# Kernel optimization log

Hardware: AMD Instinct MI355X
Metric: run time of the kernel (lower is better)

Reference implementation:

```python
import jax, jax.numpy as jnp
import numpy as np

B, S, E, H, U = 2048, 64, 512, 512, 512

def setup_inputs() -> dict:
    key = jax.random.key(0)
    ks = jax.random.split(key, 6)
    s = lambda d: 1.0 / np.sqrt(d)
    return {
        "features": jax.random.normal(ks[0], (B, S, E), jnp.float32),
        "hidden": jax.random.normal(ks[1], (B, H), jnp.float32),
        "W1": jax.random.normal(ks[2], (E, U), jnp.float32) * s(E),
        "b1": jnp.zeros((U,), jnp.float32),
        "W2": jax.random.normal(ks[3], (H, U), jnp.float32) * s(H),
        "b2": jnp.zeros((U,), jnp.float32),
        "Wv": jax.random.normal(ks[4], (U, 1), jnp.float32) * s(U),
        "bv": jnp.zeros((1,), jnp.float32),
    }

def reference(features, hidden, W1, b1, W2, b2, Wv, bv):
    # Bahdanau additive attention (dropout at inference = identity).
    h1 = jnp.einsum('bse,eu->bsu', features, W1) + b1          # [B,S,U]
    h2 = hidden @ W2 + b2                                       # [B,U]
    scores = jnp.tanh(h1 + h2[:, None, :]) @ Wv + bv            # [B,S,1]
    weights = jax.nn.softmax(scores, axis=1)                    # softmax over seq
    context = jnp.sum(weights * features, axis=1)               # [B,E]
    return context
```

## Files before the change

### kernel.cpp

```cpp
#include <hip/hip_runtime.h>

typedef _Float16 f16x8 __attribute__((ext_vector_type(8)));
typedef unsigned short u16x4 __attribute__((ext_vector_type(4)));
typedef float f32x4 __attribute__((ext_vector_type(4)));

#define VMWAIT(N) asm volatile("s_waitcnt vmcnt(" #N ")" ::: "memory")

__global__ void convert_w_kernel(const float* __restrict__ w1,
                                 const float* __restrict__ w2,
                                 unsigned short* __restrict__ w1img,
                                 unsigned short* __restrict__ w2img) {
    int u = blockIdx.x;
    int k = threadIdx.x + blockIdx.y * 256;
    size_t idx = (size_t)(k >> 5) * 16384 + (size_t)u * 32 + (k & 31);
    _Float16 h1 = (_Float16)w1[(size_t)k * 512 + u];
    _Float16 h2 = (_Float16)w2[(size_t)k * 512 + u];
    w1img[idx] = __builtin_bit_cast(unsigned short, h1);
    w2img[idx] = __builtin_bit_cast(unsigned short, h2);
}

__device__ __forceinline__ void stage_a64(const float* __restrict__ src,
                                          char* As, int tid) {
    const int row = tid >> 2, q = tid & 3;
    const float* p = src + (size_t)row * 512 + q * 4;
    const int sw2 = ((row >> 1) & 3) << 4;
    char* wb = As + row * 64;
    float4 va[4], vb[4];
#define AISS(V, G) { _Pragma("unroll") \
    for (int j_ = 0; j_ < 4; ++j_) V[j_] = *(const float4*)(p + ((G) * 4 + j_) * 16); }
#define APRC(V, G) { _Pragma("unroll") \
    for (int j_ = 0; j_ < 4; ++j_) { \
        const int i_ = (G) * 4 + j_; \
        u16x4 h_; \
        h_[0] = __builtin_bit_cast(unsigned short, (_Float16)V[j_].x); \
        h_[1] = __builtin_bit_cast(unsigned short, (_Float16)V[j_].y); \
        h_[2] = __builtin_bit_cast(unsigned short, (_Float16)V[j_].z); \
        h_[3] = __builtin_bit_cast(unsigned short, (_Float16)V[j_].w); \
        *(u16x4*)(wb + (i_ >> 1) * 4096 + ((q * 8 + (i_ & 1) * 32) ^ sw2)) = h_; } }
    AISS(va, 0); AISS(vb, 1);
    VMWAIT(4); APRC(va, 0); AISS(va, 2);
    VMWAIT(4); APRC(vb, 1); AISS(vb, 3);
    VMWAIT(4); APRC(va, 2); AISS(va, 4);
    VMWAIT(4); APRC(vb, 3); AISS(vb, 5);
    VMWAIT(4); APRC(va, 4); AISS(va, 6);
    VMWAIT(4); APRC(vb, 5); AISS(vb, 7);
    VMWAIT(4); APRC(va, 6);
    VMWAIT(0); APRC(vb, 7);
#undef AISS
#undef APRC
}

__device__ __forceinline__ void chunk_gemm(const char* __restrict__ bcol,
                                           const char* As, const int* aoff,
                                           f32x4 acc[4][4]) {
    f16x8 brA[4], brB[4], afA[4], afB[4];
    #pragma unroll
    for (int i = 0; i < 4; ++i)
        #pragma unroll
        for (int j = 0; j < 4; ++j) acc[i][j] = (f32x4){0.f, 0.f, 0.f, 0.f};
    #pragma unroll
    for (int j = 0; j < 4; ++j) brA[j] = *(const f16x8*)(bcol + j * 1024);
    #pragma unroll
    for (int j = 0; j < 4; ++j) brB[j] = *(const f16x8*)(bcol + 32768 + j * 1024);
    #pragma unroll
    for (int i = 0; i < 4; ++i) afA[i] = *(const f16x8*)(As + aoff[i]);

    #pragma unroll
    for (int tt = 0; tt < 8; ++tt) {
        const int t0 = 2 * tt, t1 = t0 + 1;
        if (t0 < 15) {
            #pragma unroll
            for (int i = 0; i < 4; ++i)
                afB[i] = *(const f16x8*)(As + t1 * 4096 + aoff[i]);
        }
        VMWAIT(4);
        #pragma unroll
        for (int i = 0; i < 4; ++i)
            #pragma unroll
            for (int j = 0; j < 4; ++j)
                acc[i][j] = __builtin_amdgcn_mfma_f32_16x16x32_f16(afA[i], brA[j], acc[i][j], 0, 0, 0);
        if (t0 < 14) {
            #pragma unroll
            for (int j = 0; j < 4; ++j)
                brA[j] = *(const f16x8*)(bcol + (t0 + 2) * 32768 + j * 1024);
        }
        if (t1 < 15) {
            #pragma unroll
            for (int i = 0; i < 4; ++i)
                afA[i] = *(const f16x8*)(As + (t1 + 1) * 4096 + aoff[i]);
        }
        if (t1 < 14) { VMWAIT(4); } else { VMWAIT(0); }
        #pragma unroll
        for (int i = 0; i < 4; ++i)
            #pragma unroll
            for (int j = 0; j < 4; ++j)
                acc[i][j] = __builtin_amdgcn_mfma_f32_16x16x32_f16(afB[i], brB[j], acc[i][j], 0, 0, 0);
        if (t1 < 14) {
            #pragma unroll
            for (int j = 0; j < 4; ++j)
                brB[j] = *(const f16x8*)(bcol + (t1 + 2) * 32768 + j * 1024);
        }
    }
}

__global__ __launch_bounds__(256, 2)
void h2_gemm_kernel(const float* __restrict__ hidden,
                    const char* __restrict__ w2img,
                    const float* __restrict__ b2,
                    float* __restrict__ h2o) {
    __shared__ char As[65536];
    const int tid = threadIdx.x, bm = blockIdx.x;
    const int lane = tid & 63, wid = tid >> 6;
    const int lane16 = lane & 15, g = lane >> 4;
    stage_a64(hidden + (size_t)bm * 32768, As, tid);
    __syncthreads();
    const int swA = (lane16 >> 1) & 3;
    int aoff[4];
    #pragma unroll
    for (int i = 0; i < 4; ++i)
        aoff[i] = (i * 16 + lane16) * 64 + ((g ^ swA) << 4);
    #pragma unroll
    for (int c = 0; c < 2; ++c) {
        const char* bcol = w2img + (size_t)(wid * 128 + c * 64 + lane16) * 64 + g * 16;
        f32x4 acc[4][4];
        chunk_gemm(bcol, As, aoff, acc);
        #pragma unroll
        for (int j = 0; j < 4; ++j) {
            int col = wid * 128 + c * 64 + j * 16 + lane16;
            float bb = b2[col];
            #pragma unroll
            for (int i = 0; i < 4; ++i)
                #pragma unroll
                for (int r = 0; r < 4; ++r)
                    h2o[(size_t)(bm * 64 + i * 16 + g * 4 + r) * 512 + col] = acc[i][j][r] + bb;
        }
    }
}

__global__ __launch_bounds__(256, 2)
void fused_all_kernel(const float* __restrict__ feat,
                      const char* __restrict__ w1img,
                      const float* __restrict__ h2,
                      const float* __restrict__ b1,
                      const float* __restrict__ wv,
                      float* __restrict__ out) {
    __shared__ char As[65536];
    __shared__ float spl[256];
    __shared__ float wsm[64];
    const int tid = threadIdx.x, bm = blockIdx.x;
    const int lane = tid & 63, wid = tid >> 6;
    const int lane16 = lane & 15, g = lane >> 4;

    stage_a64(feat + (size_t)bm * 32768, As, tid);
    __syncthreads();

    float hhv[8], wvv[8];
    #pragma unroll
    for (int j = 0; j < 8; ++j) {
        int u = wid * 128 + j * 16 + lane16;
        hhv[j] = b1[u] + h2[(size_t)bm * 512 + u];
        wvv[j] = wv[u];
    }
    VMWAIT(0);

    const int swA = (lane16 >> 1) & 3;
    int aoff[4];
    #pragma unroll
    for (int i = 0; i < 4; ++i)
        aoff[i] = (i * 16 + lane16) * 64 + ((g ^ swA) << 4);

    float sacc[16];
    #pragma unroll
    for (int x = 0; x < 16; ++x) sacc[x] = 0.f;

    #pragma unroll
    for (int c = 0; c < 2; ++c) {
        const char* bcol = w1img + (size_t)(wid * 128 + c * 64 + lane16) * 64 + g * 16;
        f32x4 acc[4][4];
        chunk_gemm(bcol, As, aoff, acc);
        #pragma unroll
        for (int i = 0; i < 4; ++i)
            #pragma unroll
            for (int r = 0; r < 4; ++r) {
                float s = 0.f;
                #pragma unroll
                for (int j = 0; j < 4; ++j) {
                    float h = acc[i][j][r] + hhv[c * 4 + j];
                    float ex = __expf(2.f * h);
                    s += (1.f - 2.f * __builtin_amdgcn_rcpf(ex + 1.f)) * wvv[c * 4 + j];
                }
                sacc[i * 4 + r] += s;
            }
    }

    #pragma unroll
    for (int i = 0; i < 4; ++i)
        #pragma unroll
        for (int r = 0; r < 4; ++r) {
            float s = sacc[i * 4 + r];
            s += __shfl_xor(s, 1); s += __shfl_xor(s, 2);
            s += __shfl_xor(s, 4); s += __shfl_xor(s, 8);
            if (lane16 == 0) spl[(i * 16 + g * 4 + r) * 4 + wid] = s;
        }
    __syncthreads();

    if (tid < 64) {
        float s = (spl[tid * 4 + 0] + spl[tid * 4 + 1]) +
                  (spl[tid * 4 + 2] + spl[tid * 4 + 3]);
        float m = s;
        #pragma unroll
        for (int off = 32; off; off >>= 1) m = fmaxf(m, __shfl_xor(m, off));
        float e = __expf(s - m);
        float sum = e;
        #pragma unroll
        for (int off = 32; off; off >>= 1) sum += __shfl_xor(sum, off);
        wsm[tid] = e / sum;
    }
    __syncthreads();

    {
        const int cseg = (tid >> 4) * 4096;
        const int cin = (tid & 15) * 4;
        float ax = 0.f, ay = 0.f;
        #pragma unroll 8
        for (int s = 0; s < 64; ++s) {
            unsigned v = *(const unsigned*)(As + cseg + s * 64 +
                                            (cin ^ (((s >> 1) & 3) << 4)));
            float w = wsm[s];
            ax += w * (float)__builtin_bit_cast(_Float16, (unsigned short)(v & 0xffffu));
            ay += w * (float)__builtin_bit_cast(_Float16, (unsigned short)(v >> 16));
        }
        ((float2*)out)[(size_t)bm * 256 + tid] = make_float2(ax, ay);
    }
}

extern "C" void kernel_launch(void* const* d_in, const int* in_sizes, int n_in,
                              void* d_out, int out_size, void* d_ws, size_t ws_size,
                              hipStream_t stream) {
    (void)in_sizes; (void)n_in; (void)out_size; (void)ws_size;
    const float* feat   = (const float*)d_in[0];
    const float* hidden = (const float*)d_in[1];
    const float* W1     = (const float*)d_in[2];
    const float* b1     = (const float*)d_in[3];
    const float* W2     = (const float*)d_in[4];
    const float* b2     = (const float*)d_in[5];
    const float* Wv     = (const float*)d_in[6];
    float* out = (float*)d_out;

    char* ws = (char*)d_ws;
    unsigned short* w1img = (unsigned short*)(ws);
    unsigned short* w2img = (unsigned short*)(ws + 524288);
    float* h2 = (float*)(ws + 1048576);

    convert_w_kernel<<<dim3(512, 2), dim3(256), 0, stream>>>(W1, W2, w1img, w2img);
    h2_gemm_kernel<<<dim3(32), dim3(256), 0, stream>>>(hidden, (const char*)w2img, b2, h2);
    fused_all_kernel<<<dim3(2048), dim3(256), 0, stream>>>(feat, (const char*)w1img, h2, b1, Wv, out);
}
```

Before: 149.6 us.

## Rewrite fused attention as persistent 8-batch pipeline with async LDS ring

The fused kernel now runs 256 blocks of 512 threads, each handling 8 batches in sequence. Raw fp32 feature tiles stream into a 128KB LDS ring via global_load_lds and are converted to fp16 in registers just before the MFMA, while W1 fragments are prefetched three k-steps ahead. This is meant to overlap feature loading with compute and remove the separate staging phase. The context sum now re-reads fp32 features from global memory in the exact precision. The h2 GEMM is also split across a second grid dimension for more parallelism. Risks include lower occupancy from the large LDS footprint, a barrier on every k-step, and the extra global reads in the context pass.

```diff
diff --git a/kernel.cpp b/kernel.cpp
--- a/kernel.cpp
+++ b/kernel.cpp
@@ -1,10 +1,30 @@
 #include <hip/hip_runtime.h>
 
 typedef _Float16 f16x8 __attribute__((ext_vector_type(8)));
+typedef __fp16 fp16x2 __attribute__((ext_vector_type(2)));
 typedef unsigned short u16x4 __attribute__((ext_vector_type(4)));
 typedef float f32x4 __attribute__((ext_vector_type(4)));
 
 #define VMWAIT(N) asm volatile("s_waitcnt vmcnt(" #N ")" ::: "memory")
+#define LGKM0()   asm volatile("s_waitcnt lgkmcnt(0)" ::: "memory")
+#define FENCE()   asm volatile("" ::: "memory")
+#define RBAR()    do { FENCE(); __builtin_amdgcn_s_barrier(); FENCE(); } while (0)
+
+__device__ __forceinline__ void gload_lds16(const void* gsrc, void* ldst) {
+    __builtin_amdgcn_global_load_lds(
+        (const unsigned int __attribute__((address_space(1)))*)gsrc,
+        (unsigned int __attribute__((address_space(3)))*)ldst,
+        16, 0, 0);
+}
+
+__device__ __forceinline__ u16x4 cvt4(float4 v) {
+    u16x4 h;
+    h[0] = __builtin_bit_cast(unsigned short, (_Float16)v.x);
+    h[1] = __builtin_bit_cast(unsigned short, (_Float16)v.y);
+    h[2] = __builtin_bit_cast(unsigned short, (_Float16)v.z);
+    h[3] = __builtin_bit_cast(unsigned short, (_Float16)v.w);
+    return h;
+}
 
 __global__ void convert_w_kernel(const float* __restrict__ w1,
                                  const float* __restrict__ w2,
@@ -31,12 +51,7 @@
 #define APRC(V, G) { _Pragma("unroll") \
     for (int j_ = 0; j_ < 4; ++j_) { \
         const int i_ = (G) * 4 + j_; \
-        u16x4 h_; \
-        h_[0] = __builtin_bit_cast(unsigned short, (_Float16)V[j_].x); \
-        h_[1] = __builtin_bit_cast(unsigned short, (_Float16)V[j_].y); \
-        h_[2] = __builtin_bit_cast(unsigned short, (_Float16)V[j_].z); \
-        h_[3] = __builtin_bit_cast(unsigned short, (_Float16)V[j_].w); \
-        *(u16x4*)(wb + (i_ >> 1) * 4096 + ((q * 8 + (i_ & 1) * 32) ^ sw2)) = h_; } }
+        *(u16x4*)(wb + (i_ >> 1) * 4096 + ((q * 8 + (i_ & 1) * 32) ^ sw2)) = cvt4(V[j_]); } }
     AISS(va, 0); AISS(vb, 1);
     VMWAIT(4); APRC(va, 0); AISS(va, 2);
     VMWAIT(4); APRC(vb, 1); AISS(vb, 3);
@@ -64,15 +79,12 @@
     for (int j = 0; j < 4; ++j) brB[j] = *(const f16x8*)(bcol + 32768 + j * 1024);
     #pragma unroll
     for (int i = 0; i < 4; ++i) afA[i] = *(const f16x8*)(As + aoff[i]);
-
     #pragma unroll
     for (int tt = 0; tt < 8; ++tt) {
         const int t0 = 2 * tt, t1 = t0 + 1;
-        if (t0 < 15) {
-            #pragma unroll
-            for (int i = 0; i < 4; ++i)
-                afB[i] = *(const f16x8*)(As + t1 * 4096 + aoff[i]);
-        }
+        #pragma unroll
+        for (int i = 0; i < 4; ++i)
+            afB[i] = *(const f16x8*)(As + t1 * 4096 + aoff[i]);
         VMWAIT(4);
         #pragma unroll
         for (int i = 0; i < 4; ++i)
@@ -109,75 +121,136 @@
                     const float* __restrict__ b2,
                     float* __restrict__ h2o) {
     __shared__ char As[65536];
-    const int tid = threadIdx.x, bm = blockIdx.x;
+    const int tid = threadIdx.x, bm = blockIdx.x, bn = blockIdx.y;
     const int lane = tid & 63, wid = tid >> 6;
     const int lane16 = lane & 15, g = lane >> 4;
     stage_a64(hidden + (size_t)bm * 32768, As, tid);
     __syncthreads();
-    const int swA = (lane16 >> 1) & 3;
     int aoff[4];
     #pragma unroll
     for (int i = 0; i < 4; ++i)
-        aoff[i] = (i * 16 + lane16) * 64 + ((g ^ swA) << 4);
-    #pragma unroll
-    for (int c = 0; c < 2; ++c) {
-        const char* bcol = w2img + (size_t)(wid * 128 + c * 64 + lane16) * 64 + g * 16;
-        f32x4 acc[4][4];
-        chunk_gemm(bcol, As, aoff, acc);
-        #pragma unroll
-        for (int j = 0; j < 4; ++j) {
-            int col = wid * 128 + c * 64 + j * 16 + lane16;
-            float bb = b2[col];
-            #pragma unroll
-            for (int i = 0; i < 4; ++i)
-                #pragma unroll
-                for (int r = 0; r < 4; ++r)
-                    h2o[(size_t)(bm * 64 + i * 16 + g * 4 + r) * 512 + col] = acc[i][j][r] + bb;
-        }
-    }
-}
-
-__global__ __launch_bounds__(256, 2)
+        aoff[i] = (i * 16 + lane16) * 64 + ((g ^ ((lane16 >> 1) & 3)) << 4);
+    const char* bcol = w2img + (size_t)(bn * 256 + wid * 64 + lane16) * 64 + g * 16;
+    f32x4 acc[4][4];
+    chunk_gemm(bcol, As, aoff, acc);
+    #pragma unroll
+    for (int j = 0; j < 4; ++j) {
+        int col = bn * 256 + wid * 64 + j * 16 + lane16;
+        float bb = b2[col];
+        #pragma unroll
+        for (int i = 0; i < 4; ++i)
+            #pragma unroll
+            for (int r = 0; r < 4; ++r)
+                h2o[(size_t)(bm * 64 + i * 16 + g * 4 + r) * 512 + col] = acc[i][j][r] + bb;
+    }
+}
+
+__global__ __launch_bounds__(512, 2)
 void fused_all_kernel(const float* __restrict__ feat,
                       const char* __restrict__ w1img,
                       const float* __restrict__ h2,
                       const float* __restrict__ b1,
                       const float* __restrict__ wv,
                       float* __restrict__ out) {
-    __shared__ char As[65536];
-    __shared__ float spl[256];
+    __shared__ char ring[131072];
+    __shared__ float hhs[8 * 512];
+    __shared__ float wvs[512];
+    __shared__ float spl[64 * 8];
     __shared__ float wsm[64];
-    const int tid = threadIdx.x, bm = blockIdx.x;
-    const int lane = tid & 63, wid = tid >> 6;
-    const int lane16 = lane & 15, g = lane >> 4;
-
-    stage_a64(feat + (size_t)bm * 32768, As, tid);
-    __syncthreads();
-
-    float hhv[8], wvv[8];
-    #pragma unroll
-    for (int j = 0; j < 8; ++j) {
-        int u = wid * 128 + j * 16 + lane16;
-        hhv[j] = b1[u] + h2[(size_t)bm * 512 + u];
-        wvv[j] = wv[u];
-    }
+
+    const int tid = threadIdx.x;
+    const int lane16 = tid & 15, g = (tid >> 4) & 3;
+    const int wid = tid >> 6;
+    const int b0 = blockIdx.x * 8;
+    const int r7 = lane16 & 7;
+
+    {
+        float bb = b1[tid];
+        wvs[tid] = wv[tid];
+        #pragma unroll
+        for (int it = 0; it < 8; ++it)
+            hhs[it * 512 + tid] = bb + h2[(size_t)(b0 + it) * 512 + tid];
+    }
+    const int arow = tid >> 3, aslot = tid & 7;
+    const size_t asrc0 = (size_t)arow * 2048 + ((size_t)(aslot ^ (arow & 7)) << 4);
+    const char* fb = (const char*)feat;
+
     VMWAIT(0);
-
-    const int swA = (lane16 >> 1) & 3;
-    int aoff[4];
-    #pragma unroll
-    for (int i = 0; i < 4; ++i)
-        aoff[i] = (i * 16 + lane16) * 64 + ((g ^ swA) << 4);
-
-    float sacc[16];
-    #pragma unroll
-    for (int x = 0; x < 16; ++x) sacc[x] = 0.f;
-
-    #pragma unroll
-    for (int c = 0; c < 2; ++c) {
-        const char* bcol = w1img + (size_t)(wid * 128 + c * 64 + lane16) * 64 + g * 16;
+    FENCE();
+    #pragma unroll
+    for (int u = 0; u < 12; ++u)
+        gload_lds16(fb + (size_t)b0 * 131072 + (size_t)u * 128 + asrc0,
+                    ring + u * 8192 + tid * 16);
+    FENCE();
+    f16x8 bf[4][4];
+    #pragma unroll
+    for (int q = 0; q < 3; ++q) {
+        #pragma unroll
+        for (int j = 0; j < 4; ++j)
+            bf[q][j] = *(const f16x8*)(w1img + (size_t)q * 32768 +
+                        (size_t)(wid * 64 + j * 16 + lane16) * 64 + g * 16);
+        FENCE();
+    }
+    LGKM0();
+    RBAR();
+
+    #pragma unroll 1
+    for (int it = 0; it < 8; ++it) {
         f32x4 acc[4][4];
-        chunk_gemm(bcol, As, aoff, acc);
+        #pragma unroll
+        for (int i = 0; i < 4; ++i)
+            #pragma unroll
+            for (int j = 0; j < 4; ++j) acc[i][j] = (f32x4){0.f, 0.f, 0.f, 0.f};
+        float hhv[4], wvv[4];
+        #pragma unroll
+        for (int j = 0; j < 4; ++j) {
+            int col = wid * 64 + j * 16 + lane16;
+            hhv[j] = hhs[it * 512 + col];
+            wvv[j] = wvs[col];
+        }
+
+        #pragma unroll
+        for (int t = 0; t < 16; ++t) {
+            VMWAIT(10);
+            RBAR();
+            f16x8 af[4];
+            #pragma unroll
+            for (int i = 0; i < 4; ++i) {
+                const char* base = ring + t * 8192 + (i * 16 + lane16) * 128;
+                float4 lo = *(const float4*)(base + (((2 * g + 0) ^ r7) << 4));
+                float4 hi = *(const float4*)(base + (((2 * g + 1) ^ r7) << 4));
+                union { fp16x2 p[4]; f16x8 v; } uu;
+                uu.p[0] = __builtin_amdgcn_cvt_pkrtz(lo.x, lo.y);
+                uu.p[1] = __builtin_amdgcn_cvt_pkrtz(lo.z, lo.w);
+                uu.p[2] = __builtin_amdgcn_cvt_pkrtz(hi.x, hi.y);
+                uu.p[3] = __builtin_amdgcn_cvt_pkrtz(hi.z, hi.w);
+                af[i] = uu.v;
+            }
+            __builtin_amdgcn_s_setprio(1);
+            #pragma unroll
+            for (int i = 0; i < 4; ++i)
+                #pragma unroll
+                for (int j = 0; j < 4; ++j)
+                    acc[i][j] = __builtin_amdgcn_mfma_f32_16x16x32_f16(af[i], bf[t & 3][j], acc[i][j], 0, 0, 0);
+            __builtin_amdgcn_s_setprio(0);
+            FENCE();
+            {
+                const int u_ = (t + 12) & 15;
+                const int bn = b0 + ((it + (t >= 4 ? 1 : 0)) & 7);
+                gload_lds16(fb + (size_t)bn * 131072 + (size_t)u_ * 128 + asrc0,
+                            ring + u_ * 8192 + tid * 16);
+            }
+            FENCE();
+            {
+                const int q = (t + 3) & 3, kt = (t + 3) & 15;
+                #pragma unroll
+                for (int j = 0; j < 4; ++j)
+                    bf[q][j] = *(const f16x8*)(w1img + (size_t)kt * 32768 +
+                                (size_t)(wid * 64 + j * 16 + lane16) * 64 + g * 16);
+            }
+            FENCE();
+        }
+
         #pragma unroll
         for (int i = 0; i < 4; ++i)
             #pragma unroll
@@ -185,52 +258,60 @@
                 float s = 0.f;
                 #pragma unroll
                 for (int j = 0; j < 4; ++j) {
-                    float h = acc[i][j][r] + hhv[c * 4 + j];
+                    float h = acc[i][j][r] + hhv[j];
                     float ex = __expf(2.f * h);
-                    s += (1.f - 2.f * __builtin_amdgcn_rcpf(ex + 1.f)) * wvv[c * 4 + j];
+                    s += (1.f - 2.f * __builtin_amdgcn_rcpf(ex + 1.f)) * wvv[j];
                 }
-                sacc[i * 4 + r] += s;
+                s += __shfl_xor(s, 1); s += __shfl_xor(s, 2);
+                s += __shfl_xor(s, 4); s += __shfl_xor(s, 8);
+                if (lane16 == 0) spl[(i * 16 + g * 4 + r) * 8 + wid] = s;
             }
-    }
-
-    #pragma unroll
-    for (int i = 0; i < 4; ++i)
-        #pragma unroll
-        for (int r = 0; r < 4; ++r) {
-            float s = sacc[i * 4 + r];
-            s += __shfl_xor(s, 1); s += __shfl_xor(s, 2);
-            s += __shfl_xor(s, 4); s += __shfl_xor(s, 8);
-            if (lane16 == 0) spl[(i * 16 + g * 4 + r) * 4 + wid] = s;
-        }
-    __syncthreads();
-
-    if (tid < 64) {
-        float s = (spl[tid * 4 + 0] + spl[tid * 4 + 1]) +
-                  (spl[tid * 4 + 2] + spl[tid * 4 + 3]);
-        float m = s;
-        #pragma unroll
-        for (int off = 32; off; off >>= 1) m = fmaxf(m, __shfl_xor(m, off));
-        float e = __expf(s - m);
-        float sum = e;
-        #pragma unroll
-        for (int off = 32; off; off >>= 1) sum += __shfl_xor(sum, off);
-        wsm[tid] = e / sum;
-    }
-    __syncthreads();
-
-    {
-        const int cseg = (tid >> 4) * 4096;
-        const int cin = (tid & 15) * 4;
-        float ax = 0.f, ay = 0.f;
-        #pragma unroll 8
-        for (int s = 0; s < 64; ++s) {
-            unsigned v = *(const unsigned*)(As + cseg + s * 64 +
-                                            (cin ^ (((s >> 1) & 3) << 4)));
-            float w = wsm[s];
-            ax += w * (float)__builtin_bit_cast(_Float16, (unsigned short)(v & 0xffffu));
-            ay += w * (float)__builtin_bit_cast(_Float16, (unsigned short)(v >> 16));
-        }
-        ((float2*)out)[(size_t)bm * 256 + tid] = make_float2(ax, ay);
+        LGKM0();
+        RBAR();
+        if (tid < 64) {
+            float s = ((spl[tid * 8 + 0] + spl[tid * 8 + 1]) + (spl[tid * 8 + 2] + spl[tid * 8 + 3])) +
+                      ((spl[tid * 8 + 4] + spl[tid * 8 + 5]) + (spl[tid * 8 + 6] + spl[tid * 8 + 7]));
+            float m = s;
+            #pragma unroll
+            for (int off = 32; off; off >>= 1) m = fmaxf(m, __shfl_xor(m, off));
+            float e = __expf(s - m);
+            float sum = e;
+            #pragma unroll
+            for (int off = 32; off; off >>= 1) sum += __shfl_xor(sum, off);
+            wsm[tid] = e / sum;
+        }
+        LGKM0();
+        RBAR();
+        {
+            const float* fr = feat + (size_t)(b0 + it) * 32768 + tid;
+            float v0[16], v1[16], a = 0.f;
+            #pragma unroll
+            for (int s2 = 0; s2 < 16; ++s2) v0[s2] = fr[s2 * 512];
+            FENCE();
+            #pragma unroll
+            for (int s2 = 0; s2 < 16; ++s2) v1[s2] = fr[(16 + s2) * 512];
+            FENCE();
+            VMWAIT(16);
+            #pragma unroll
+            for (int s2 = 0; s2 < 16; ++s2) a += wsm[s2] * v0[s2];
+            #pragma unroll
+            for (int s2 = 0; s2 < 16; ++s2) v0[s2] = fr[(32 + s2) * 512];
+            FENCE();
+            VMWAIT(16);
+            #pragma unroll
+            for (int s2 = 0; s2 < 16; ++s2) a += wsm[16 + s2] * v1[s2];
+            #pragma unroll
+            for (int s2 = 0; s2 < 16; ++s2) v1[s2] = fr[(48 + s2) * 512];
+            FENCE();
+            VMWAIT(16);
+            #pragma unroll
+            for (int s2 = 0; s2 < 16; ++s2) a += wsm[32 + s2] * v0[s2];
+            VMWAIT(0);
+            #pragma unroll
+            for (int s2 = 0; s2 < 16; ++s2) a += wsm[48 + s2] * v1[s2];
+            out[(size_t)(b0 + it) * 512 + tid] = a;
+        }
+        FENCE();
     }
 }
 
@@ -253,6 +334,6 @@
     float* h2 = (float*)(ws + 1048576);
 
     convert_w_kernel<<<dim3(512, 2), dim3(256), 0, stream>>>(W1, W2, w1img, w2img);
-    h2_gemm_kernel<<<dim3(32), dim3(256), 0, stream>>>(hidden, (const char*)w2img, b2, h2);
-    fused_all_kernel<<<dim3(2048), dim3(256), 0, stream>>>(feat, (const char*)w1img, h2, b1, Wv, out);
-}
+    h2_gemm_kernel<<<dim3(32, 2), dim3(256), 0, stream>>>(hidden, (const char*)w2img, b2, h2);
+    fused_all_kernel<<<dim3(256), dim3(512), 0, stream>>>(feat, (const char*)w1img, h2, b1, Wv, out);
+}
```

New measurement: 291.9 us. 95.2% more time.
